# Performance work log

Hardware: AMD Instinct MI355X
Metric: run time of the kernel (lower is better)

The kernel has to match this reference:

```python
import jax, jax.numpy as jnp
import numpy as np

MAX_ITER = 10
EPS = 1e-5

def _weight_quant(w):
    # BitNet b1.58 ternary weight quant: scale by mean |w|, round-clip to {-1,0,1}
    gamma = jnp.clip(jnp.mean(jnp.abs(w)), EPS, None)
    return jnp.clip(jnp.round(w / gamma), -1.0, 1.0) * gamma

def _act_quant(x):
    # per-token absmax 8-bit activation quant
    scale = 127.0 / jnp.clip(jnp.max(jnp.abs(x), axis=-1, keepdims=True), EPS, None)
    return jnp.clip(jnp.round(x * scale), -128.0, 127.0) / scale

def _bitlinear(x, w, b):
    xq = _act_quant(x)
    wq = _weight_quant(w)
    return xq @ wq.T + b

def setup_inputs() -> dict:
    key = jax.random.key(0)
    k_x, k_w1, k_w2 = jax.random.split(key, 3)
    features, intermediate, tokens = 4096, 16384, 4096
    x = jax.random.normal(k_x, (tokens, features), dtype=jnp.float32)
    s1 = 1.0 / np.sqrt(features)
    s2 = 1.0 / np.sqrt(intermediate)
    W1 = jax.random.uniform(k_w1, (intermediate, features), jnp.float32, -s1, s1)
    b1 = jnp.zeros((intermediate,), jnp.float32)
    W2 = jax.random.uniform(k_w2, (features, intermediate), jnp.float32, -s2, s2)
    b2 = jnp.zeros((features,), jnp.float32)
    return {"x": x, "W1": W1, "b1": b1, "W2": W2, "b2": b2}

def reference(x, W1, b1, W2, b2):
    # Euler integration: x <- x + net(x)/max_iter, fixed max_iter steps
    # (early-exit torch.allclose only fires in eval when dx==0; omitted here)
    inv = 1.0 / MAX_ITER
    def step(i, x):
        h = jax.nn.silu(_bitlinear(x, W1, b1))
        dx = _bitlinear(h, W2, b2)
        return x + dx * inv
    return jax.lax.fori_loop(0, MAX_ITER, step, x)
```

## Files before the change

### kernel.cpp

```cpp
#include <hip/hip_runtime.h>
#include <hip/hip_bf16.h>

typedef __bf16 bf16_t;
typedef __bf16 bf16x8 __attribute__((ext_vector_type(8)));
typedef float f32x4 __attribute__((ext_vector_type(4)));

#define MAX_ITER 10
#define EPSQ 1e-5f


__device__ static inline unsigned short f2bf(float f) {
    union { __bf16 b; unsigned short u; } cvt;
    cvt.b = (__bf16)f;
    return cvt.u;
}

__device__ static inline void gload16(const void* g, void* l) {
    __builtin_amdgcn_global_load_lds((const __attribute__((address_space(1))) void*)g,
                                     (__attribute__((address_space(3))) void*)l,
                                     16, 0, 0);
}


__global__ __launch_bounds__(256) void absum_kernel(const float* __restrict__ W,
                                                    long n4, double* __restrict__ out) {
    double s = 0.0;
    const float4* w4 = (const float4*)W;
    for (long i = (long)blockIdx.x * 256 + threadIdx.x; i < n4; i += (long)gridDim.x * 256) {
        float4 v = w4[i];
        s += (double)(fabsf(v.x) + fabsf(v.y) + fabsf(v.z) + fabsf(v.w));
    }
#pragma unroll
    for (int off = 32; off > 0; off >>= 1) s += __shfl_xor(s, off);
    __shared__ double wsum[4];
    const int wid = threadIdx.x >> 6;
    if ((threadIdx.x & 63) == 0) wsum[wid] = s;
    __syncthreads();
    if (threadIdx.x == 0) atomicAdd(out, wsum[0] + wsum[1] + wsum[2] + wsum[3]);
}


__global__ __launch_bounds__(256) void wquant_kernel(const float* __restrict__ W,
                                                     bf16_t* __restrict__ Q, long n4,
                                                     const double* __restrict__ gsum,
                                                     double invcnt) {
    const float gamma = fmaxf((float)(gsum[0] * invcnt), EPSQ);
    const float4* w4 = (const float4*)W;
    ushort4* q4 = (ushort4*)Q;
    for (long i = (long)blockIdx.x * 256 + threadIdx.x; i < n4; i += (long)gridDim.x * 256) {
        float4 v = w4[i];
        ushort4 o;
        o.x = f2bf(fminf(fmaxf(rintf(v.x / gamma), -1.f), 1.f));
        o.y = f2bf(fminf(fmaxf(rintf(v.y / gamma), -1.f), 1.f));
        o.z = f2bf(fminf(fmaxf(rintf(v.z / gamma), -1.f), 1.f));
        o.w = f2bf(fminf(fmaxf(rintf(v.w / gamma), -1.f), 1.f));
        q4[i] = o;
    }
}


template <int NV>
__global__ __launch_bounds__(256) void actquant_kernel(const float* __restrict__ X,
                                                       bf16_t* __restrict__ Q,
                                                       float* __restrict__ rscale, int L) {
    const int row = blockIdx.x;
    const float4* xr = (const float4*)(X + (size_t)row * L);
    float4 v[NV];
    float am = 0.f;
#pragma unroll
    for (int i = 0; i < NV; i++) {
        v[i] = xr[threadIdx.x + i * 256];
        am = fmaxf(am, fmaxf(fmaxf(fabsf(v[i].x), fabsf(v[i].y)),
                             fmaxf(fabsf(v[i].z), fabsf(v[i].w))));
    }
#pragma unroll
    for (int off = 32; off > 0; off >>= 1) am = fmaxf(am, __shfl_xor(am, off));
    __shared__ float wmax[4];
    const int wid = threadIdx.x >> 6;
    if ((threadIdx.x & 63) == 0) wmax[wid] = am;
    __syncthreads();
    am = fmaxf(fmaxf(wmax[0], wmax[1]), fmaxf(wmax[2], wmax[3]));
    const float scale = 127.f / fmaxf(am, EPSQ);
    if (threadIdx.x == 0) rscale[row] = scale;
    ushort4* qr = (ushort4*)(Q + (size_t)row * L);
#pragma unroll
    for (int i = 0; i < NV; i++) {
        ushort4 o;
        o.x = f2bf(fminf(fmaxf(rintf(v[i].x * scale), -128.f), 127.f));
        o.y = f2bf(fminf(fmaxf(rintf(v[i].y * scale), -128.f), 127.f));
        o.z = f2bf(fminf(fmaxf(rintf(v[i].z * scale), -128.f), 127.f));
        o.w = f2bf(fminf(fmaxf(rintf(v[i].w * scale), -128.f), 127.f));
        qr[threadIdx.x + i * 256] = o;
    }
}


template <int EPI>
__global__ __launch_bounds__(256) void gemm_bt(const bf16_t* __restrict__ A,
                                               const bf16_t* __restrict__ B,
                                               int M, int N, int K,
                                               const float* __restrict__ rowScale,
                                               const double* __restrict__ gsum, double invcnt,
                                               const float* __restrict__ bias,
                                               float* __restrict__ out,
                                               const float* __restrict__ xin, float euler) {
    constexpr int BM = 128, BN = 128, BK = 32;
    __shared__ bf16_t As[BM * BK];
    __shared__ bf16_t Bs[BN * BK];
    const int tid = threadIdx.x;
    const int wid = tid >> 6, lane = tid & 63;
    const int wr = wid >> 1, wc = wid & 1;
    const int Mt = M / BM;
    const int mt = blockIdx.x % Mt, nt = blockIdx.x / Mt;

    const int c0 = tid, c1 = tid + 256;
    const bf16_t* Ag0 = A + (size_t)(mt * BM + (c0 >> 2)) * K + (c0 & 3) * 8;
    const bf16_t* Ag1 = A + (size_t)(mt * BM + (c1 >> 2)) * K + (c1 & 3) * 8;
    const bf16_t* Bg0 = B + (size_t)(nt * BN + (c0 >> 2)) * K + (c0 & 3) * 8;
    const bf16_t* Bg1 = B + (size_t)(nt * BN + (c1 >> 2)) * K + (c1 & 3) * 8;
    char* AsW0 = (char*)As + wid * 1024;
    char* AsW1 = (char*)As + 4096 + wid * 1024;
    char* BsW0 = (char*)Bs + wid * 1024;
    char* BsW1 = (char*)Bs + 4096 + wid * 1024;

    const bf16x8* Ard = (const bf16x8*)(As + (wr * 64 + (lane & 15)) * BK + (lane >> 4) * 8);
    const bf16x8* Brd = (const bf16x8*)(Bs + (wc * 64 + (lane & 15)) * BK + (lane >> 4) * 8);

    f32x4 acc[4][4] = {};

    for (int k0 = 0; k0 < K; k0 += BK) {
        gload16(Ag0 + k0, AsW0);
        gload16(Ag1 + k0, AsW1);
        gload16(Bg0 + k0, BsW0);
        gload16(Bg1 + k0, BsW1);
        asm volatile("s_waitcnt vmcnt(0)" ::: "memory");
        __syncthreads();
        bf16x8 af[4], bq[4];
#pragma unroll
        for (int i = 0; i < 4; i++) {
            af[i] = Ard[i * 64];
            bq[i] = Brd[i * 64];
        }
#pragma unroll
        for (int i = 0; i < 4; i++)
#pragma unroll
            for (int j = 0; j < 4; j++)
                acc[i][j] = __builtin_amdgcn_mfma_f32_16x16x32_bf16(af[i], bq[j], acc[i][j], 0, 0, 0);
        __syncthreads();
    }

    const float gamma = fmaxf((float)(gsum[0] * invcnt), EPSQ);
    const int row0 = mt * BM + wr * 64 + ((lane >> 4) << 2);
    const int col0 = nt * BN + wc * 64 + (lane & 15);
#pragma unroll
    for (int i = 0; i < 4; i++) {
        float fac[4];
#pragma unroll
        for (int r = 0; r < 4; r++) fac[r] = gamma / rowScale[row0 + i * 16 + r];
#pragma unroll
        for (int j = 0; j < 4; j++) {
            const int col = col0 + j * 16;
            const float bv = bias[col];
#pragma unroll
            for (int r = 0; r < 4; r++) {
                const int row = row0 + i * 16 + r;
                const float v = acc[i][j][r] * fac[r] + bv;
                const size_t idx = (size_t)row * N + col;
                if (EPI == 0) {
                    out[idx] = v / (1.f + expf(-v));
                } else {
                    out[idx] = xin[idx] + v * euler;
                }
            }
        }
    }
}


extern "C" void kernel_launch(void* const* d_in, const int* in_sizes, int n_in,
                              void* d_out, int out_size, void* d_ws, size_t ws_size,
                              hipStream_t stream) {
    const float* x0 = (const float*)d_in[0];
    const float* W1 = (const float*)d_in[1];
    const float* b1 = (const float*)d_in[2];
    const float* W2 = (const float*)d_in[3];
    const float* b2 = (const float*)d_in[4];

    const int I = in_sizes[2];
    const int F = in_sizes[4];
    const int M = in_sizes[0] / F;
    const long nW = (long)I * F;

    char* ws = (char*)d_ws;
    double* gsum = (double*)ws;
    float* xscale = (float*)(ws + 256);
    float* hscale = xscale + M;
    size_t off = 256 + 2 * (size_t)M * 4;
    off = (off + 255) & ~(size_t)255;
    bf16_t* Xq = (bf16_t*)(ws + off);  off += (size_t)M * F * 2;
    bf16_t* Hq = (bf16_t*)(ws + off);  off += (size_t)M * I * 2;
    bf16_t* W1q = (bf16_t*)(ws + off); off += (size_t)nW * 2;
    bf16_t* W2q = (bf16_t*)(ws + off); off += (size_t)nW * 2;
    float* h = (float*)(ws + off);     off += (size_t)M * I * 4;
    (void)ws_size; (void)n_in; (void)out_size;

    float* x = (float*)d_out;
    hipMemcpyAsync(x, x0, (size_t)M * F * 4, hipMemcpyDeviceToDevice, stream);
    hipMemsetAsync(gsum, 0, 16, stream);

    absum_kernel<<<2048, 256, 0, stream>>>(W1, nW / 4, gsum + 0);
    absum_kernel<<<2048, 256, 0, stream>>>(W2, nW / 4, gsum + 1);
    wquant_kernel<<<2048, 256, 0, stream>>>(W1, W1q, nW / 4, gsum + 0, 1.0 / (double)nW);
    wquant_kernel<<<2048, 256, 0, stream>>>(W2, W2q, nW / 4, gsum + 1, 1.0 / (double)nW);

    const float euler = 1.0f / (float)MAX_ITER;
    for (int it = 0; it < MAX_ITER; ++it) {
        actquant_kernel<4><<<M, 256, 0, stream>>>(x, Xq, xscale, F);
        gemm_bt<0><<<(M / 128) * (I / 128), 256, 0, stream>>>(
            Xq, W1q, M, I, F, xscale, gsum + 0, 1.0 / (double)nW, b1, h, nullptr, 0.f);
        actquant_kernel<16><<<M, 256, 0, stream>>>(h, Hq, hscale, I);
        gemm_bt<1><<<(M / 128) * (F / 128), 256, 0, stream>>>(
            Hq, W2q, M, F, I, hscale, gsum + 1, 1.0 / (double)nW, b2, x, x, euler);
    }
}
```

Measured before the change: 19.57 ms.

## Double-buffer LDS in GEMM and remap blocks for XCD and tile locality

The GEMM kernel now keeps two LDS buffers and issues the global-to-LDS loads for the next K tile before computing the current one. The wait is relaxed to vmcnt(4), so memory latency overlaps with the MFMA work instead of stalling every iteration. Block IDs are also remapped so each XCD gets a contiguous range, and tiles are grouped into 4x4 supertiles to improve L2 reuse. LDS use doubles, and the remap assumes the M tile count is divisible by 4 and that the grid splits evenly into groups of 16.

```diff
diff --git a/kernel.cpp b/kernel.cpp
--- a/kernel.cpp
+++ b/kernel.cpp
@@ -105,36 +105,45 @@
                                                float* __restrict__ out,
                                                const float* __restrict__ xin, float euler) {
     constexpr int BM = 128, BN = 128, BK = 32;
-    __shared__ bf16_t As[BM * BK];
-    __shared__ bf16_t Bs[BN * BK];
+    __shared__ bf16_t As[2][BM * BK];
+    __shared__ bf16_t Bs[2][BN * BK];
     const int tid = threadIdx.x;
     const int wid = tid >> 6, lane = tid & 63;
     const int wr = wid >> 1, wc = wid & 1;
+
+    const int nwg = gridDim.x;
+    int bid = blockIdx.x;
+    const int q = nwg >> 3, r = nwg & 7;
+    const int xcd = bid & 7, boff = bid >> 3;
+    bid = (xcd < r ? xcd * (q + 1) : r * (q + 1) + (xcd - r) * q) + boff;
     const int Mt = M / BM;
-    const int mt = blockIdx.x % Mt, nt = blockIdx.x / Mt;
+    const int Mt4 = Mt >> 2;
+    const int sup = bid >> 4, wi = bid & 15;
+    const int mt = (sup % Mt4) * 4 + (wi & 3);
+    const int nt = (sup / Mt4) * 4 + (wi >> 2);
 
     const int c0 = tid, c1 = tid + 256;
     const bf16_t* Ag0 = A + (size_t)(mt * BM + (c0 >> 2)) * K + (c0 & 3) * 8;
     const bf16_t* Ag1 = A + (size_t)(mt * BM + (c1 >> 2)) * K + (c1 & 3) * 8;
     const bf16_t* Bg0 = B + (size_t)(nt * BN + (c0 >> 2)) * K + (c0 & 3) * 8;
     const bf16_t* Bg1 = B + (size_t)(nt * BN + (c1 >> 2)) * K + (c1 & 3) * 8;
-    char* AsW0 = (char*)As + wid * 1024;
-    char* AsW1 = (char*)As + 4096 + wid * 1024;
-    char* BsW0 = (char*)Bs + wid * 1024;
-    char* BsW1 = (char*)Bs + 4096 + wid * 1024;
-
-    const bf16x8* Ard = (const bf16x8*)(As + (wr * 64 + (lane & 15)) * BK + (lane >> 4) * 8);
-    const bf16x8* Brd = (const bf16x8*)(Bs + (wc * 64 + (lane & 15)) * BK + (lane >> 4) * 8);
+    char* AsB = (char*)As;
+    char* BsB = (char*)Bs;
 
     f32x4 acc[4][4] = {};
-
-    for (int k0 = 0; k0 < K; k0 += BK) {
-        gload16(Ag0 + k0, AsW0);
-        gload16(Ag1 + k0, AsW1);
-        gload16(Bg0 + k0, BsW0);
-        gload16(Bg1 + k0, BsW1);
-        asm volatile("s_waitcnt vmcnt(0)" ::: "memory");
-        __syncthreads();
+    const int NT = K / BK;
+
+    auto stage = [&](int buf, int k0) {
+        char* ad = AsB + buf * 8192 + wid * 1024;
+        char* bd = BsB + buf * 8192 + wid * 1024;
+        gload16(Ag0 + k0, ad);
+        gload16(Ag1 + k0, ad + 4096);
+        gload16(Bg0 + k0, bd);
+        gload16(Bg1 + k0, bd + 4096);
+    };
+    auto compute = [&](int buf) {
+        const bf16x8* Ard = (const bf16x8*)(As[buf] + (wr * 64 + (lane & 15)) * BK + (lane >> 4) * 8);
+        const bf16x8* Brd = (const bf16x8*)(Bs[buf] + (wc * 64 + (lane & 15)) * BK + (lane >> 4) * 8);
         bf16x8 af[4], bq[4];
 #pragma unroll
         for (int i = 0; i < 4; i++) {
@@ -146,8 +155,22 @@
 #pragma unroll
             for (int j = 0; j < 4; j++)
                 acc[i][j] = __builtin_amdgcn_mfma_f32_16x16x32_bf16(af[i], bq[j], acc[i][j], 0, 0, 0);
-        __syncthreads();
-    }
+    };
+
+    stage(0, 0);
+    for (int t = 0; t < NT - 1; ++t) {
+        stage((t + 1) & 1, (t + 1) * BK);
+        asm volatile("s_waitcnt vmcnt(4)" ::: "memory");
+        __builtin_amdgcn_s_barrier();
+        __builtin_amdgcn_sched_barrier(0);
+        compute(t & 1);
+        __builtin_amdgcn_sched_barrier(0);
+        __builtin_amdgcn_s_barrier();
+    }
+    asm volatile("s_waitcnt vmcnt(0)" ::: "memory");
+    __builtin_amdgcn_s_barrier();
+    __builtin_amdgcn_sched_barrier(0);
+    compute((NT - 1) & 1);
 
     const float gamma = fmaxf((float)(gsum[0] * invcnt), EPSQ);
     const int row0 = mt * BM + wr * 64 + ((lane >> 4) << 2);
@@ -156,15 +179,15 @@
     for (int i = 0; i < 4; i++) {
         float fac[4];
 #pragma unroll
-        for (int r = 0; r < 4; r++) fac[r] = gamma / rowScale[row0 + i * 16 + r];
+        for (int rr = 0; rr < 4; rr++) fac[rr] = gamma / rowScale[row0 + i * 16 + rr];
 #pragma unroll
         for (int j = 0; j < 4; j++) {
             const int col = col0 + j * 16;
             const float bv = bias[col];
 #pragma unroll
-            for (int r = 0; r < 4; r++) {
-                const int row = row0 + i * 16 + r;
-                const float v = acc[i][j][r] * fac[r] + bv;
+            for (int rr = 0; rr < 4; rr++) {
+                const int row = row0 + i * 16 + rr;
+                const float v = acc[i][j][rr] * fac[rr] + bv;
                 const size_t idx = (size_t)row * N + col;
                 if (EPI == 0) {
                     out[idx] = v / (1.f + expf(-v));
```

Result: faster. 16.14 ms (-17.5%).
